# Optimization experiments

Hardware: AMD Instinct MI355X
Metric: run time of the kernel (lower is better)

## Reference

```python
import jax, jax.numpy as jnp
import numpy as np
from jax import lax

B_, DIM, H, W, Dd = 2, 256, 16, 16, 16
DI, N, DTR, K = 256, 8, 16, 4   # d_inner (expand=1), d_state, dt_rank=ceil(256/16), d_conv
OUT_C = 1200
L = H * W * Dd
EPS = 1e-5


def setup_inputs() -> dict:
    key = jax.random.key(0)
    ks = jax.random.split(key, 20)
    g = lambda k, s: jax.random.normal(k, s, jnp.float32) * 0.02
    A_log = jnp.log(jnp.broadcast_to(jnp.arange(1, N + 1, dtype=jnp.float32), (DI, N)))
    dt_bias = jnp.full((DI,), float(np.log(np.expm1(0.01))), jnp.float32)
    return {
        "input0": jax.random.normal(ks[0], (B_, DIM, H, W, Dd), jnp.float32),
        "input1": jax.random.normal(ks[1], (B_, DIM, H, W, Dd), jnp.float32),
        "norm0_w": jnp.ones((DIM,), jnp.float32),
        "norm0_b": jnp.zeros((DIM,), jnp.float32),
        "norm1_w": jnp.ones((DIM,), jnp.float32),
        "norm1_b": jnp.zeros((DIM,), jnp.float32),
        "in_proj_w": g(ks[2], (DI, DIM)),
        "in_projz_w": g(ks[3], (DI, DIM)),
        "conv1d_w": g(ks[4], (DI, 1, K)),
        "conv1d_bias": jnp.zeros((DI,), jnp.float32),
        "conv1db_w": g(ks[5], (DI, 1, K)),
        "conv1db_bias": jnp.zeros((DI,), jnp.float32),
        "xproj_w": g(ks[6], (DTR + 2 * N, DI)),
        "xprojb_w": g(ks[7], (DTR + 2 * N, DI)),
        "dtproj_w": g(ks[8], (DI, DTR)),
        "dtproj_bias": dt_bias,
        "dtprojb_w": g(ks[9], (DI, DTR)),
        "dtprojb_bias": dt_bias,
        "A_log": A_log,
        "Ab_log": A_log,
        "D_p": jnp.ones((DI,), jnp.float32),
        "D_b": jnp.ones((DI,), jnp.float32),
        "rms_w": jnp.ones((DI,), jnp.float32),
        "out_proj_w": g(ks[10], (DIM, DI)),
        "conv3d_w": g(ks[11], (OUT_C, DIM)),
        "conv3d_bias": jnp.zeros((OUT_C,), jnp.float32),
    }


def _layernorm(x, w, b):
    m = x.mean(-1, keepdims=True)
    v = ((x - m) ** 2).mean(-1, keepdims=True)
    return (x - m) * lax.rsqrt(v + EPS) * w + b


def _rmsnorm(x, w):
    return x * lax.rsqrt((x * x).mean(-1, keepdims=True) + EPS) * w


def _ssm_dir(x, z, conv_w, conv_b, xproj_w, dtproj_w, dtproj_bias, A_log, Dp):
    # One direction of the bimamba-v2 selective scan. x, z: (b, L, d_inner)
    xt = x.transpose(0, 2, 1)  # (b, d, L)
    xc = lax.conv_general_dilated(xt, conv_w, (1,), [(K - 1, 0)], feature_group_count=DI)
    x = jax.nn.silu(xc + conv_b[None, :, None]).transpose(0, 2, 1)  # causal dw-conv + silu
    dbl = x @ xproj_w.T                                   # (b, L, dt_rank + 2n)
    dt, Bm, Cm = dbl[..., :DTR], dbl[..., DTR:DTR + N], dbl[..., DTR + N:]
    dt = jax.nn.softplus(dt @ dtproj_w.T + dtproj_bias)    # (b, L, d)
    A = -jnp.exp(A_log)                                    # (d, n)
    dA = jnp.exp(dt[..., None] * A)                        # (b, L, d, n)
    dBu = (dt * x)[..., None] * Bm[:, :, None, :]          # (b, L, d, n)

    def step(h, inp):
        dA_t, dBu_t, C_t = inp
        h = h * dA_t + dBu_t
        return h, jnp.einsum('bdn,bn->bd', h, C_t)

    h0 = jnp.zeros((x.shape[0], DI, N), x.dtype)
    _, ys = lax.scan(step, h0, (dA.transpose(1, 0, 2, 3), dBu.transpose(1, 0, 2, 3), Cm.transpose(1, 0, 2)))
    y = ys.transpose(1, 0, 2) + x * Dp                     # (b, L, d)
    return y * jax.nn.silu(z)                              # gate from the matching branch


def _forward(input0, input1, norm0_w, norm0_b, norm1_w, norm1_b, in_proj_w, in_projz_w,
             conv1d_w, conv1d_bias, conv1db_w, conv1db_bias, xproj_w, xprojb_w,
             dtproj_w, dtproj_bias, dtprojb_w, dtprojb_bias, A_log, Ab_log,
             D_p, D_b, rms_w, out_proj_w, conv3d_w, conv3d_bias):
    b = input0.shape[0]
    skip = input0
    seq0 = input0.transpose(0, 2, 3, 4, 1).reshape(b, L, DIM)  # b (h w d) c
    seq1 = input1.transpose(0, 2, 3, 4, 1).reshape(b, L, DIM)
    seq0 = _layernorm(seq0, norm0_w, norm0_b)
    seq1 = _layernorm(seq1, norm1_w, norm1_b)
    x = seq0 @ in_proj_w.T    # SSM input from input0
    z = seq1 @ in_projz_w.T   # gate from extra_emb (input1)
    y_f = _ssm_dir(x, z, conv1d_w, conv1d_bias, xproj_w, dtproj_w, dtproj_bias, A_log, D_p)
    y_b = _ssm_dir(x[:, ::-1], z[:, ::-1], conv1db_w, conv1db_bias, xprojb_w,
                   dtprojb_w, dtprojb_bias, Ab_log, D_b)[:, ::-1]

    def head(y):
        o = _rmsnorm(y, rms_w) @ out_proj_w.T              # use_norm=True, then out_proj
        o = o.reshape(b, H, W, Dd, DIM).transpose(0, 4, 1, 2, 3) + skip
        return jnp.einsum('bchwd,oc->bohwd', o, conv3d_w) + conv3d_bias[None, :, None, None, None]

    out = head((y_f + y_b) * 0.5)   # if_devide_out=True
    return out, head(y_f), head(y_b)


def reference(input0, input1, norm0_w, norm0_b, norm1_w, norm1_b, in_proj_w, in_projz_w,
              conv1d_w, conv1d_bias, conv1db_w, conv1db_bias, xproj_w, xprojb_w,
              dtproj_w, dtproj_bias, dtprojb_w, dtprojb_bias, A_log, Ab_log,
              D_p, D_b, rms_w, out_proj_w, conv3d_w, conv3d_bias):
    return _forward(input0, input1, norm0_w, norm0_b, norm1_w, norm1_b, in_proj_w, in_projz_w,
                    conv1d_w, conv1d_bias, conv1db_w, conv1db_bias, xproj_w, xprojb_w,
                    dtproj_w, dtproj_bias, dtprojb_w, dtprojb_bias, A_log, Ab_log,
                    D_p, D_b, rms_w, out_proj_w, conv3d_w, conv3d_bias)
```

## Files before the change

### kernel.cpp

```cpp
#include <hip/hip_runtime.h>
#include <cstdint>

#define NTOK 8192

typedef __attribute__((ext_vector_type(4))) float f32x4;
typedef __attribute__((ext_vector_type(8))) short s16x8;
typedef __attribute__((ext_vector_type(4))) short s16x4;

__device__ __forceinline__ short f2bf(float f) {
  union { float f; unsigned u; } x; x.f = f;
  unsigned r = x.u + 0x7FFFu + ((x.u >> 16) & 1u);
  return (short)(r >> 16);
}
__device__ __forceinline__ float bf2f(short s) {
  union { float f; unsigned u; } x;
  x.u = ((unsigned)(unsigned short)s) << 16;
  return x.f;
}
__device__ __forceinline__ void gl_lds16(const void* g, void* l) {
  __builtin_amdgcn_global_load_lds((const unsigned int*)g, (unsigned int*)l, 16, 0, 0);
}

__global__ __launch_bounds__(256) void ln_transpose_kernel(
    const float* __restrict__ in0, const float* __restrict__ in1,
    const float* __restrict__ w0, const float* __restrict__ b0,
    const float* __restrict__ w1, const float* __restrict__ b1,
    const float* __restrict__ wxp, const float* __restrict__ wzp,
    const float* __restrict__ wop, const float* __restrict__ wcp,
    short* __restrict__ Wx, short* __restrict__ Wz,
    short* __restrict__ Wo, short* __restrict__ Wc,
    short* __restrict__ xlnz)
{
  __shared__ float tile[32 * 257];
  __shared__ float mu[32], rs[32];
  const int tid  = threadIdx.x;
  const int pass = blockIdx.x >> 8;
  const int b    = (blockIdx.x >> 7) & 1;
  const int l0   = (blockIdx.x & 127) << 5;

  {
    int base = (int)blockIdx.x << 10;
    #pragma unroll
    for (int i = 0; i < 4; ++i) {
      int idx = base + (i << 8) + tid;
      if (idx < 65536)       Wx[idx] = f2bf(wxp[idx]);
      else if (idx < 131072) Wz[idx - 65536] = f2bf(wzp[idx - 65536]);
      else if (idx < 196608) Wo[idx - 131072] = f2bf(wop[idx - 131072]);
      else {
        int k = idx - 196608;
        Wc[k] = ((k >> 8) < 1200) ? f2bf(wcp[k]) : (short)0;
      }
    }
  }

  const float* in = pass ? in1 : in0;
  #pragma unroll 8
  for (int i = 0; i < 32; ++i) {
    int e = (i << 8) + tid;
    int c = e >> 5, lo = e & 31;
    tile[lo * 257 + c] = in[((size_t)(b * 256 + c) << 12) + l0 + lo];
  }
  __syncthreads();
  if (tid < 64) {
    int r = tid & 31, hh = tid >> 5;
    float s = 0.f, ss = 0.f;
    #pragma unroll 16
    for (int c = hh * 128; c < hh * 128 + 128; ++c) {
      float v = tile[r * 257 + c];
      s += v; ss += v * v;
    }
    s  += __shfl_xor(s, 32, 64);
    ss += __shfl_xor(ss, 32, 64);
    if (hh == 0) {
      float m = s * (1.f / 256.f);
      mu[r] = m;
      rs[r] = rsqrtf(ss * (1.f / 256.f) - m * m + 1e-5f);
    }
  }
  __syncthreads();
  const float* w  = pass ? w1 : w0;
  const float* bb = pass ? b1 : b0;
  float wv = w[tid], bv = bb[tid];
  #pragma unroll 8
  for (int i = 0; i < 32; ++i) {
    float v = tile[i * 257 + tid];
    int row = (pass ? 8192 : 0) + (b << 12) + l0 + i;
    xlnz[(size_t)row * 256 + tid] = f2bf((v - mu[i]) * rs[i] * wv + bv);
  }
}

template <int EPI>
__global__ __launch_bounds__(256) void gemm_fast(
    const short* __restrict__ A, const short* __restrict__ W0,
    const short* __restrict__ W1, float* __restrict__ Cf,
    short* __restrict__ Cb, const float* __restrict__ ADD,
    const float* __restrict__ bias, int Msplit)
{
  __shared__ short As[2][4096];
  __shared__ short Bs[2][4096];
  const int tid  = threadIdx.x;
  const int lane = tid & 63, wave = tid >> 6;
  const int m0 = blockIdx.y << 7;
  const int n0 = blockIdx.x << 7;
  const short* W = (EPI == 0 && m0 >= Msplit) ? W1 : W0;

  const int sr = tid >> 2;
  const int sc = (tid & 3) << 3;
  const int mf = lane & 15, kq = lane >> 4;
  const int wm = (wave & 1) << 6, wn = (wave >> 1) << 6;

  const short* Ar0 = A + (size_t)(m0 + sr) * 256 + sc;
  const short* Ar1 = A + (size_t)(m0 + 64 + sr) * 256 + sc;
  const short* Br0 = W + (size_t)(n0 + sr) * 256 + sc;
  const short* Br1 = W + (size_t)(n0 + 64 + sr) * 256 + sc;
  const int wo = wave << 9;

  f32x4 acc[4][4] = {};

  gl_lds16(Ar0, &As[0][wo]);
  gl_lds16(Ar1, &As[0][wo + 2048]);
  gl_lds16(Br0, &Bs[0][wo]);
  gl_lds16(Br1, &Bs[0][wo + 2048]);
  __syncthreads();

  #pragma unroll
  for (int t = 0; t < 8; ++t) {
    const int cur = t & 1;
    if (t < 7) {
      const int kt = (t + 1) << 5;
      gl_lds16(Ar0 + kt, &As[cur ^ 1][wo]);
      gl_lds16(Ar1 + kt, &As[cur ^ 1][wo + 2048]);
      gl_lds16(Br0 + kt, &Bs[cur ^ 1][wo]);
      gl_lds16(Br1 + kt, &Bs[cur ^ 1][wo + 2048]);
    }
    s16x8 af[4], bfr[4];
    #pragma unroll
    for (int i = 0; i < 4; ++i)
      af[i] = *(const s16x8*)&As[cur][((wm + (i << 4) + mf) << 5) + (kq << 3)];
    #pragma unroll
    for (int j = 0; j < 4; ++j)
      bfr[j] = *(const s16x8*)&Bs[cur][((wn + (j << 4) + mf) << 5) + (kq << 3)];
    #pragma unroll
    for (int i = 0; i < 4; ++i)
      #pragma unroll
      for (int j = 0; j < 4; ++j)
        acc[i][j] = __builtin_amdgcn_mfma_f32_16x16x32_bf16(af[i], bfr[j], acc[i][j], 0, 0, 0);
    __syncthreads();
  }

  if (EPI == 0) {
    #pragma unroll
    for (int i = 0; i < 4; ++i) {
      int gm = m0 + wm + (i << 4) + (kq << 2);
      #pragma unroll
      for (int j = 0; j < 4; ++j) {
        int gn = n0 + wn + (j << 4) + mf;
        #pragma unroll
        for (int r = 0; r < 4; ++r)
          Cf[(size_t)(gm + r) * 256 + gn] = acc[i][j][r];
      }
    }
  } else {
    const int head = m0 >> 13, bb = (m0 >> 12) & 1, lb = m0 & 4095;
    float* obase = Cf + (size_t)head * (2u * 1200u * 4096u) + (size_t)bb * (1200u * 4096u);
    #pragma unroll
    for (int i = 0; i < 4; ++i) {
      int l = lb + wm + (i << 4) + (kq << 2);
      #pragma unroll
      for (int j = 0; j < 4; ++j) {
        int gn = n0 + wn + (j << 4) + mf;
        if (gn < 1200) {
          float bv = bias[gn];
          f32x4 v = acc[i][j];
          v[0] += bv; v[1] += bv; v[2] += bv; v[3] += bv;
          __builtin_nontemporal_store(v, (f32x4*)&obase[(size_t)gn * 4096 + l]);
        }
      }
    }
  }
}

__global__ __launch_bounds__(256) void fused_front(
    const float* __restrict__ x,
    const float* __restrict__ cw0, const float* __restrict__ cb0,
    const float* __restrict__ cw1, const float* __restrict__ cb1,
    const float* __restrict__ xw0, const float* __restrict__ xw1,
    const float* __restrict__ dtw0, const float* __restrict__ dtb0,
    const float* __restrict__ dtw1, const float* __restrict__ dtb1,
    const float* __restrict__ Alog0, const float* __restrict__ Alog1,
    float* __restrict__ xcg, float* __restrict__ dblg,
    float* __restrict__ P, float* __restrict__ Q)
{
  __shared__ float xcs[16 * 256];
  __shared__ short wxs[32 * 264];
  __shared__ float dls[512];
  const int tid = threadIdx.x;
  const int dir = blockIdx.x >> 9;
  const int b   = (blockIdx.x >> 8) & 1;
  const int ch  = blockIdx.x & 255;
  const int t0  = ch << 4;
  const float* cw   = dir ? cw1 : cw0;
  const float* cb   = dir ? cb1 : cb0;
  const float* xw   = dir ? xw1 : xw0;
  const float* dtw  = dir ? dtw1 : dtw0;
  const float* dtb  = dir ? dtb1 : dtb0;
  const float* Alog = dir ? Alog1 : Alog0;
  const size_t dS = (size_t)dir * (NTOK * 256);
  const size_t xb = ((size_t)b) << 12;

  {
    const int d = tid;
    const float w0 = cw[(d << 2)], w1 = cw[(d << 2) + 1],
                w2 = cw[(d << 2) + 2], w3 = cw[(d << 2) + 3];
    const float bias = cb[d];
    float h0 = 0.f, h1 = 0.f, h2 = 0.f;
    #pragma unroll
    for (int i = 0; i < 3; ++i) {
      int ts = t0 - 3 + i; float v = 0.f;
      if (ts >= 0) { int tn = dir ? 4095 - ts : ts; v = x[(xb + tn) * 256 + d]; }
      h0 = h1; h1 = h2; h2 = v;
    }
    #pragma unroll
    for (int s = 0; s < 16; ++s) {
      int ts = t0 + s;
      int tn = dir ? 4095 - ts : ts;
      float xv = x[(xb + tn) * 256 + d];
      float a = bias + w0 * h0 + w1 * h1 + w2 * h2 + w3 * xv;
      h0 = h1; h1 = h2; h2 = xv;
      float v = a / (1.f + __expf(-a));
      xcs[s * 256 + d] = v;
      xcg[dS + (xb + ts) * 256 + d] = v;
    }
  }
  #pragma unroll
  for (int i = 0; i < 32; ++i)
    wxs[i * 264 + tid] = f2bf(xw[(i << 8) + tid]);
  __syncthreads();

  {
    const int j = tid & 31, s0 = tid >> 5;
    float a0 = 0.f, a1 = 0.f;
    const short* wr = &wxs[j * 264];
    const float* xa = &xcs[s0 * 256];
    const float* xbp = &xcs[(s0 + 8) * 256];
    #pragma unroll 4
    for (int rb = 0; rb < 32; ++rb) {
      s16x8 w8 = *(const s16x8*)&wr[rb << 3];
      f32x4 p0 = *(const f32x4*)&xa[rb << 3];
      f32x4 p1 = *(const f32x4*)&xa[(rb << 3) + 4];
      f32x4 q0 = *(const f32x4*)&xbp[rb << 3];
      f32x4 q1 = *(const f32x4*)&xbp[(rb << 3) + 4];
      #pragma unroll
      for (int e = 0; e < 4; ++e) {
        float w = bf2f(w8[e]);
        a0 = fmaf(p0[e], w, a0);
        a1 = fmaf(q0[e], w, a1);
      }
      #pragma unroll
      for (int e = 0; e < 4; ++e) {
        float w = bf2f(w8[4 + e]);
        a0 = fmaf(p1[e], w, a0);
        a1 = fmaf(q1[e], w, a1);
      }
    }
    dls[(s0 << 5) + j] = a0;
    dls[((s0 + 8) << 5) + j] = a1;
    size_t db = (size_t)dir * 262144 + ((xb + t0) << 5);
    dblg[db + tid] = a0;
    dblg[db + 256 + tid] = a1;
  }
  __syncthreads();

  {
    const int d = tid;
    float wrow[16];
    #pragma unroll
    for (int r = 0; r < 16; ++r) wrow[r] = dtw[(d << 4) + r];
    const float bias = dtb[d];
    float Av[8], p[8], q[8];
    #pragma unroll
    for (int n = 0; n < 8; ++n) {
      Av[n] = -expf(Alog[(d << 3) + n]); p[n] = 1.f; q[n] = 0.f;
    }
    for (int s = 0; s < 16; ++s) {
      const float* dlp = &dls[s << 5];
      f32x4 d0 = *(const f32x4*)&dlp[0];
      f32x4 d1 = *(const f32x4*)&dlp[4];
      f32x4 d2 = *(const f32x4*)&dlp[8];
      f32x4 d3 = *(const f32x4*)&dlp[12];
      float a = bias;
      #pragma unroll
      for (int e = 0; e < 4; ++e) a = fmaf(d0[e], wrow[e], a);
      #pragma unroll
      for (int e = 0; e < 4; ++e) a = fmaf(d1[e], wrow[4 + e], a);
      #pragma unroll
      for (int e = 0; e < 4; ++e) a = fmaf(d2[e], wrow[8 + e], a);
      #pragma unroll
      for (int e = 0; e < 4; ++e) a = fmaf(d3[e], wrow[12 + e], a);
      float dtv = (a > 20.f) ? a : log1pf(__expf(a));
      float xv = xcs[s * 256 + d];
      float du = dtv * xv;
      float Bv[8];
      *(f32x4*)&Bv[0] = *(const f32x4*)&dlp[16];
      *(f32x4*)&Bv[4] = *(const f32x4*)&dlp[20];
      #pragma unroll
      for (int n = 0; n < 8; ++n) {
        float dA = __expf(dtv * Av[n]);
        p[n] *= dA;
        q[n] = fmaf(q[n], dA, du * Bv[n]);
      }
    }
    size_t ob = (size_t)dir * 1048576 + ((size_t)((b << 8) + ch) * 8) * 256 + d;
    #pragma unroll
    for (int n = 0; n < 8; ++n) { P[ob + (n << 8)] = p[n]; Q[ob + (n << 8)] = q[n]; }
  }
}

__global__ __launch_bounds__(64) void scan_p2(
    const float* __restrict__ P, const float* __restrict__ Q, float* __restrict__ Hs)
{
  const int d   = ((blockIdx.x & 3) << 6) + threadIdx.x;
  const int bid = blockIdx.x >> 2;
  const int dir = bid >> 4, b = (bid >> 3) & 1, n = bid & 7;
  const size_t dOff = (size_t)dir * 1048576;
  float h = 0.f;
  #pragma unroll 8
  for (int ch = 0; ch < 256; ++ch) {
    size_t i = dOff + ((size_t)((b << 8) + ch) * 8 + n) * 256 + d;
    Hs[i] = h;
    h = fmaf(P[i], h, Q[i]);
  }
}

__global__ __launch_bounds__(256) void scan_p3(
    const float* __restrict__ xcg, const float* __restrict__ dblg,
    const float* __restrict__ dtw0, const float* __restrict__ dtb0,
    const float* __restrict__ dtw1, const float* __restrict__ dtb1,
    const float* __restrict__ Hs, const float* __restrict__ z,
    const float* __restrict__ Alog0, const float* __restrict__ Alog1,
    const float* __restrict__ Dp0, const float* __restrict__ Dp1,
    short* __restrict__ yall)
{
  __shared__ float dl[512];
  const int d = threadIdx.x;
  const int dir = blockIdx.x >> 9;
  const int b   = (blockIdx.x >> 8) & 1;
  const int ch  = blockIdx.x & 255;
  const int t0  = ch << 4;
  const float* dtw  = dir ? dtw1 : dtw0;
  const float* dtb  = dir ? dtb1 : dtb0;
  const float* Alog = dir ? Alog1 : Alog0;
  const float* Dp   = dir ? Dp1 : Dp0;
  const size_t dS = (size_t)dir * (NTOK * 256);
  const size_t xb = ((size_t)b) << 12;
  short* y = yall + (size_t)dir * (NTOK * 256);

  size_t db = (size_t)dir * 262144 + ((xb + t0) << 5);
  dl[d]       = dblg[db + d];
  dl[256 + d] = dblg[db + 256 + d];
  float wrow[16];
  #pragma unroll
  for (int r = 0; r < 16; ++r) wrow[r] = dtw[(d << 4) + r];
  const float bias = dtb[d];
  float Av[8], h[8];
  #pragma unroll
  for (int n = 0; n < 8; ++n) Av[n] = -expf(Alog[(d << 3) + n]);
  size_t hb = (size_t)dir * 1048576 + ((size_t)((b << 8) + ch) * 8) * 256 + d;
  #pragma unroll
  for (int n = 0; n < 8; ++n) h[n] = Hs[hb + (n << 8)];
  const float Dv = Dp[d];
  __syncthreads();
  for (int s = 0; s < 16; ++s) {
    const float* dlp = &dl[s << 5];
    f32x4 d0 = *(const f32x4*)&dlp[0];
    f32x4 d1 = *(const f32x4*)&dlp[4];
    f32x4 d2 = *(const f32x4*)&dlp[8];
    f32x4 d3 = *(const f32x4*)&dlp[12];
    float a = bias;
    #pragma unroll
    for (int e = 0; e < 4; ++e) a = fmaf(d0[e], wrow[e], a);
    #pragma unroll
    for (int e = 0; e < 4; ++e) a = fmaf(d1[e], wrow[4 + e], a);
    #pragma unroll
    for (int e = 0; e < 4; ++e) a = fmaf(d2[e], wrow[8 + e], a);
    #pragma unroll
    for (int e = 0; e < 4; ++e) a = fmaf(d3[e], wrow[12 + e], a);
    float dtv = (a > 20.f) ? a : log1pf(__expf(a));
    int ts = t0 + s;
    float xv = xcg[dS + (xb + ts) * 256 + d];
    float du = dtv * xv;
    float Bv[8], Cv[8];
    *(f32x4*)&Bv[0] = *(const f32x4*)&dlp[16];
    *(f32x4*)&Bv[4] = *(const f32x4*)&dlp[20];
    *(f32x4*)&Cv[0] = *(const f32x4*)&dlp[24];
    *(f32x4*)&Cv[4] = *(const f32x4*)&dlp[28];
    float yv = 0.f;
    #pragma unroll
    for (int n = 0; n < 8; ++n) {
      float dA = __expf(dtv * Av[n]);
      h[n] = fmaf(h[n], dA, du * Bv[n]);
      yv = fmaf(h[n], Cv[n], yv);
    }
    yv = fmaf(xv, Dv, yv);
    int tn = dir ? (4095 - ts) : ts;
    size_t zi = (xb + tn) * 256 + d;
    float zv = z[zi];
    y[zi] = f2bf(yv * zv / (1.f + __expf(-zv)));
  }
}

__global__ __launch_bounds__(256) void gemm_rms_epi1(
    const short* __restrict__ yall, const short* __restrict__ W0,
    const float* __restrict__ rmsw, short* __restrict__ Cb,
    const float* __restrict__ in0)
{
  __shared__ short As[2048];
  __shared__ short Bs[4096];
  __shared__ float scale[64];
  __shared__ float rw[256];
  const int tid  = threadIdx.x;
  const int lane = tid & 63, wave = tid >> 6;
  const int m0 = blockIdx.y << 6;
  const int n0 = blockIdx.x << 7;
  const int mode = m0 >> 13;
  const int tok0 = m0 & 8191;
  const short* yf = yall;
  const short* yb = yall + 2097152;
  const short* ysel = (mode == 1) ? yf : yb;

  rw[tid] = rmsw[tid];

  for (int rr = 0; rr < 16; ++rr) {
    int r = (rr << 2) + wave;
    size_t base = (size_t)(tok0 + r) * 256 + (lane << 2);
    float v0, v1, v2, v3;
    if (mode == 0) {
      s16x4 a = *(const s16x4*)&yf[base];
      s16x4 c = *(const s16x4*)&yb[base];
      v0 = 0.5f * (bf2f(a[0]) + bf2f(c[0]));
      v1 = 0.5f * (bf2f(a[1]) + bf2f(c[1]));
      v2 = 0.5f * (bf2f(a[2]) + bf2f(c[2]));
      v3 = 0.5f * (bf2f(a[3]) + bf2f(c[3]));
    } else {
      s16x4 a = *(const s16x4*)&ysel[base];
      v0 = bf2f(a[0]); v1 = bf2f(a[1]); v2 = bf2f(a[2]); v3 = bf2f(a[3]);
    }
    float ss = v0 * v0 + v1 * v1 + v2 * v2 + v3 * v3;
    #pragma unroll
    for (int o = 32; o > 0; o >>= 1) ss += __shfl_xor(ss, o, 64);
    if (lane == 0) scale[r] = rsqrtf(ss * (1.f / 256.f) + 1e-5f);
  }
  __syncthreads();

  const int sr = tid >> 2;
  const int sc = (tid & 3) << 3;
  const int mf = lane & 15, kq = lane >> 4;
  const int wn = wave << 5;
  const short* Br0 = W0 + (size_t)(n0 + sr) * 256 + sc;
  const short* Br1 = W0 + (size_t)(n0 + 64 + sr) * 256 + sc;
  const int wo = wave << 9;

  const int ar = tid >> 2;
  const int ac = (tid & 3) << 3;
  const size_t abase = (size_t)(tok0 + ar) * 256 + ac;
  const float s_r = scale[ar];

  f32x4 acc[4][2] = {};

  for (int t = 0; t < 8; ++t) {
    const int kt = t << 5;
    {
      s16x8 o0;
      if (mode == 0) {
        s16x8 f0 = *(const s16x8*)&yf[abase + kt];
        s16x8 c0 = *(const s16x8*)&yb[abase + kt];
        #pragma unroll
        for (int e = 0; e < 8; ++e)
          o0[e] = f2bf((0.5f * (bf2f(f0[e]) + bf2f(c0[e])) * s_r) * rw[kt + ac + e]);
      } else {
        s16x8 f0 = *(const s16x8*)&ysel[abase + kt];
        #pragma unroll
        for (int e = 0; e < 8; ++e)
          o0[e] = f2bf((bf2f(f0[e]) * s_r) * rw[kt + ac + e]);
      }
      *(s16x8*)&As[(ar << 5) + ac] = o0;
    }
    gl_lds16(Br0 + kt, &Bs[wo]);
    gl_lds16(Br1 + kt, &Bs[wo + 2048]);
    __syncthreads();
    s16x8 af[4], bfr[2];
    #pragma unroll
    for (int i = 0; i < 4; ++i)
      af[i] = *(const s16x8*)&As[(((i << 4) + mf) << 5) + (kq << 3)];
    #pragma unroll
    for (int j = 0; j < 2; ++j)
      bfr[j] = *(const s16x8*)&Bs[((wn + (j << 4) + mf) << 5) + (kq << 3)];
    #pragma unroll
    for (int i = 0; i < 4; ++i)
      #pragma unroll
      for (int j = 0; j < 2; ++j)
        acc[i][j] = __builtin_amdgcn_mfma_f32_16x16x32_bf16(af[i], bfr[j], acc[i][j], 0, 0, 0);
    __syncthreads();
  }

  #pragma unroll
  for (int i = 0; i < 4; ++i) {
    int gm = m0 + (i << 4) + (kq << 2);
    int tok = gm & 8191;
    int bb2 = tok >> 12, ll = tok & 4095;
    #pragma unroll
    for (int j = 0; j < 2; ++j) {
      int gn = n0 + wn + (j << 4) + mf;
      f32x4 sk = *(const f32x4*)&in0[((((size_t)(bb2 << 8)) + gn) << 12) + ll];
      #pragma unroll
      for (int r = 0; r < 4; ++r) {
        float v = acc[i][j][r] + sk[r];
        Cb[(size_t)(gm + r) * 256 + gn] = f2bf(v);
      }
    }
  }
}

extern "C" void kernel_launch(void* const* d_in, const int* in_sizes, int n_in,
                              void* d_out, int out_size, void* d_ws, size_t ws_size,
                              hipStream_t stream) {
  const float* in0        = (const float*)d_in[0];
  const float* in1        = (const float*)d_in[1];
  const float* n0w        = (const float*)d_in[2];
  const float* n0b        = (const float*)d_in[3];
  const float* n1w        = (const float*)d_in[4];
  const float* n1b        = (const float*)d_in[5];
  const float* in_proj_w  = (const float*)d_in[6];
  const float* in_projz_w = (const float*)d_in[7];
  const float* conv1d_w   = (const float*)d_in[8];
  const float* conv1d_b   = (const float*)d_in[9];
  const float* conv1db_w  = (const float*)d_in[10];
  const float* conv1db_b  = (const float*)d_in[11];
  const float* xproj_w    = (const float*)d_in[12];
  const float* xprojb_w   = (const float*)d_in[13];
  const float* dtproj_w   = (const float*)d_in[14];
  const float* dtproj_b   = (const float*)d_in[15];
  const float* dtprojb_w  = (const float*)d_in[16];
  const float* dtprojb_b  = (const float*)d_in[17];
  const float* A_log      = (const float*)d_in[18];
  const float* Ab_log     = (const float*)d_in[19];
  const float* D_p        = (const float*)d_in[20];
  const float* D_b        = (const float*)d_in[21];
  const float* rms_w      = (const float*)d_in[22];
  const float* out_proj_w = (const float*)d_in[23];
  const float* conv3d_w   = (const float*)d_in[24];
  const float* conv3d_b   = (const float*)d_in[25];
  (void)in_sizes; (void)n_in; (void)out_size; (void)ws_size;

  float* ws = (float*)d_ws;
  size_t o = 0;
  short* xlnz = (short*)(ws + o); o += 2097152;
  float* x    = ws + o;           o += 2097152;
  float* z    = ws + o;           o += 2097152;
  float* xc2  = ws + o;           o += 4194304;
  float* dbl2 = ws + o;           o += 524288;
  float* P    = ws + o;           o += 2097152;
  float* Q    = ws + o;           o += 2097152;
  float* Hs   = ws + o;           o += 2097152;
  short* yall = (short*)(ws + o); o += 2097152;
  short* obuf = (short*)(ws + o); o += 3145728;
  short* Wx   = (short*)(ws + o); o += 32768;
  short* Wz   = (short*)(ws + o); o += 32768;
  short* Wo   = (short*)(ws + o); o += 32768;
  short* Wc   = (short*)(ws + o); o += 163840;
  float* out  = (float*)d_out;

  dim3 blk(256);

  ln_transpose_kernel<<<dim3(512), blk, 0, stream>>>(
      in0, in1, n0w, n0b, n1w, n1b,
      in_proj_w, in_projz_w, out_proj_w, conv3d_w, Wx, Wz, Wo, Wc,
      xlnz);

  gemm_fast<0><<<dim3(2, 128), blk, 0, stream>>>(xlnz, Wx, Wz, x, nullptr, nullptr, nullptr, 8192);

  fused_front<<<dim3(1024), blk, 0, stream>>>(
      x, conv1d_w, conv1d_b, conv1db_w, conv1db_b,
      xproj_w, xprojb_w, dtproj_w, dtproj_b, dtprojb_w, dtprojb_b,
      A_log, Ab_log, xc2, dbl2, P, Q);

  scan_p2<<<dim3(128), dim3(64), 0, stream>>>(P, Q, Hs);

  scan_p3<<<dim3(1024), blk, 0, stream>>>(
      xc2, dbl2, dtproj_w, dtproj_b, dtprojb_w, dtprojb_b,
      Hs, z, A_log, Ab_log, D_p, D_b, yall);

  gemm_rms_epi1<<<dim3(2, 384), blk, 0, stream>>>(yall, Wo, rms_w, obuf, in0);
  gemm_fast<2><<<dim3(10, 192), blk, 0, stream>>>(obuf, Wc, nullptr, out, nullptr, nullptr, conv3d_b, 0);
}
```

Measured before the change: 333.5 us.

## Fuse three RMS-norm heads into one GEMM pass; use smaller M tiles for in_proj

The out_proj GEMM now handles all three heads (averaged, forward, backward) in one block per token tile. It reads yf and yb once, builds three normalized A tiles, and reuses each loaded weight tile across three accumulator sets. Before, three separate row ranges each reloaded y and the weights. The in_proj GEMM is split into a 64-row-tile kernel so the launch has twice as many blocks and fills the CUs better. The cost is higher register and LDS use per block in the fused kernel, which may lower occupancy.

```diff
diff --git a/kernel.cpp b/kernel.cpp
--- a/kernel.cpp
+++ b/kernel.cpp
@@ -89,12 +89,75 @@
   }
 }
 
-template <int EPI>
-__global__ __launch_bounds__(256) void gemm_fast(
+__global__ __launch_bounds__(256) void gemm_in64(
     const short* __restrict__ A, const short* __restrict__ W0,
-    const short* __restrict__ W1, float* __restrict__ Cf,
-    short* __restrict__ Cb, const float* __restrict__ ADD,
-    const float* __restrict__ bias, int Msplit)
+    const short* __restrict__ W1, float* __restrict__ Cf, int Msplit)
+{
+  __shared__ short As[2][2048];
+  __shared__ short Bs[2][4096];
+  const int tid  = threadIdx.x;
+  const int lane = tid & 63, wave = tid >> 6;
+  const int m0 = blockIdx.y << 6;
+  const int n0 = blockIdx.x << 7;
+  const short* W = (m0 >= Msplit) ? W1 : W0;
+
+  const int sr = tid >> 2;
+  const int sc = (tid & 3) << 3;
+  const int mf = lane & 15, kq = lane >> 4;
+  const int wn = wave << 5;
+
+  const short* Ar  = A + (size_t)(m0 + sr) * 256 + sc;
+  const short* Br0 = W + (size_t)(n0 + sr) * 256 + sc;
+  const short* Br1 = W + (size_t)(n0 + 64 + sr) * 256 + sc;
+  const int wo = wave << 9;
+
+  f32x4 acc[4][2] = {};
+
+  gl_lds16(Ar, &As[0][wo]);
+  gl_lds16(Br0, &Bs[0][wo]);
+  gl_lds16(Br1, &Bs[0][wo + 2048]);
+  __syncthreads();
+
+  #pragma unroll
+  for (int t = 0; t < 8; ++t) {
+    const int cur = t & 1;
+    if (t < 7) {
+      const int kt = (t + 1) << 5;
+      gl_lds16(Ar + kt, &As[cur ^ 1][wo]);
+      gl_lds16(Br0 + kt, &Bs[cur ^ 1][wo]);
+      gl_lds16(Br1 + kt, &Bs[cur ^ 1][wo + 2048]);
+    }
+    s16x8 af[4], bfr[2];
+    #pragma unroll
+    for (int i = 0; i < 4; ++i)
+      af[i] = *(const s16x8*)&As[cur][(((i << 4) + mf) << 5) + (kq << 3)];
+    #pragma unroll
+    for (int j = 0; j < 2; ++j)
+      bfr[j] = *(const s16x8*)&Bs[cur][((wn + (j << 4) + mf) << 5) + (kq << 3)];
+    #pragma unroll
+    for (int i = 0; i < 4; ++i)
+      #pragma unroll
+      for (int j = 0; j < 2; ++j)
+        acc[i][j] = __builtin_amdgcn_mfma_f32_16x16x32_bf16(af[i], bfr[j], acc[i][j], 0, 0, 0);
+    __syncthreads();
+  }
+
+  #pragma unroll
+  for (int i = 0; i < 4; ++i) {
+    int gm = m0 + (i << 4) + (kq << 2);
+    #pragma unroll
+    for (int j = 0; j < 2; ++j) {
+      int gn = n0 + wn + (j << 4) + mf;
+      #pragma unroll
+      for (int r = 0; r < 4; ++r)
+        Cf[(size_t)(gm + r) * 256 + gn] = acc[i][j][r];
+    }
+  }
+}
+
+__global__ __launch_bounds__(256) void gemm_conv3d(
+    const short* __restrict__ A, const short* __restrict__ W0,
+    float* __restrict__ Cf, const float* __restrict__ bias)
 {
   __shared__ short As[2][4096];
   __shared__ short Bs[2][4096];
@@ -102,7 +165,6 @@
   const int lane = tid & 63, wave = tid >> 6;
   const int m0 = blockIdx.y << 7;
   const int n0 = blockIdx.x << 7;
-  const short* W = (EPI == 0 && m0 >= Msplit) ? W1 : W0;
 
   const int sr = tid >> 2;
   const int sc = (tid & 3) << 3;
@@ -111,8 +173,8 @@
 
   const short* Ar0 = A + (size_t)(m0 + sr) * 256 + sc;
   const short* Ar1 = A + (size_t)(m0 + 64 + sr) * 256 + sc;
-  const short* Br0 = W + (size_t)(n0 + sr) * 256 + sc;
-  const short* Br1 = W + (size_t)(n0 + 64 + sr) * 256 + sc;
+  const short* Br0 = W0 + (size_t)(n0 + sr) * 256 + sc;
+  const short* Br1 = W0 + (size_t)(n0 + 64 + sr) * 256 + sc;
   const int wo = wave << 9;
 
   f32x4 acc[4][4] = {};
@@ -148,33 +210,19 @@
     __syncthreads();
   }
 
-  if (EPI == 0) {
-    #pragma unroll
-    for (int i = 0; i < 4; ++i) {
-      int gm = m0 + wm + (i << 4) + (kq << 2);
-      #pragma unroll
-      for (int j = 0; j < 4; ++j) {
-        int gn = n0 + wn + (j << 4) + mf;
-        #pragma unroll
-        for (int r = 0; r < 4; ++r)
-          Cf[(size_t)(gm + r) * 256 + gn] = acc[i][j][r];
-      }
-    }
-  } else {
-    const int head = m0 >> 13, bb = (m0 >> 12) & 1, lb = m0 & 4095;
-    float* obase = Cf + (size_t)head * (2u * 1200u * 4096u) + (size_t)bb * (1200u * 4096u);
-    #pragma unroll
-    for (int i = 0; i < 4; ++i) {
-      int l = lb + wm + (i << 4) + (kq << 2);
-      #pragma unroll
-      for (int j = 0; j < 4; ++j) {
-        int gn = n0 + wn + (j << 4) + mf;
-        if (gn < 1200) {
-          float bv = bias[gn];
-          f32x4 v = acc[i][j];
-          v[0] += bv; v[1] += bv; v[2] += bv; v[3] += bv;
-          __builtin_nontemporal_store(v, (f32x4*)&obase[(size_t)gn * 4096 + l]);
-        }
+  const int head = m0 >> 13, bb = (m0 >> 12) & 1, lb = m0 & 4095;
+  float* obase = Cf + (size_t)head * (2u * 1200u * 4096u) + (size_t)bb * (1200u * 4096u);
+  #pragma unroll
+  for (int i = 0; i < 4; ++i) {
+    int l = lb + wm + (i << 4) + (kq << 2);
+    #pragma unroll
+    for (int j = 0; j < 4; ++j) {
+      int gn = n0 + wn + (j << 4) + mf;
+      if (gn < 1200) {
+        float bv = bias[gn];
+        f32x4 v = acc[i][j];
+        v[0] += bv; v[1] += bv; v[2] += bv; v[3] += bv;
+        __builtin_nontemporal_store(v, (f32x4*)&obase[(size_t)gn * 4096 + l]);
       }
     }
   }
@@ -409,46 +457,47 @@
   }
 }
 
-__global__ __launch_bounds__(256) void gemm_rms_epi1(
+__global__ __launch_bounds__(256) void gemm_rms3(
     const short* __restrict__ yall, const short* __restrict__ W0,
     const float* __restrict__ rmsw, short* __restrict__ Cb,
     const float* __restrict__ in0)
 {
-  __shared__ short As[2048];
+  __shared__ short As0[2048], As1[2048], As2[2048];
   __shared__ short Bs[4096];
-  __shared__ float scale[64];
+  __shared__ float sc0[64], sc1[64], sc2[64];
   __shared__ float rw[256];
   const int tid  = threadIdx.x;
   const int lane = tid & 63, wave = tid >> 6;
-  const int m0 = blockIdx.y << 6;
+  const int tok0 = blockIdx.y << 6;
   const int n0 = blockIdx.x << 7;
-  const int mode = m0 >> 13;
-  const int tok0 = m0 & 8191;
   const short* yf = yall;
   const short* yb = yall + 2097152;
-  const short* ysel = (mode == 1) ? yf : yb;
 
   rw[tid] = rmsw[tid];
 
   for (int rr = 0; rr < 16; ++rr) {
     int r = (rr << 2) + wave;
     size_t base = (size_t)(tok0 + r) * 256 + (lane << 2);
-    float v0, v1, v2, v3;
-    if (mode == 0) {
-      s16x4 a = *(const s16x4*)&yf[base];
-      s16x4 c = *(const s16x4*)&yb[base];
-      v0 = 0.5f * (bf2f(a[0]) + bf2f(c[0]));
-      v1 = 0.5f * (bf2f(a[1]) + bf2f(c[1]));
-      v2 = 0.5f * (bf2f(a[2]) + bf2f(c[2]));
-      v3 = 0.5f * (bf2f(a[3]) + bf2f(c[3]));
-    } else {
-      s16x4 a = *(const s16x4*)&ysel[base];
-      v0 = bf2f(a[0]); v1 = bf2f(a[1]); v2 = bf2f(a[2]); v3 = bf2f(a[3]);
-    }
-    float ss = v0 * v0 + v1 * v1 + v2 * v2 + v3 * v3;
-    #pragma unroll
-    for (int o = 32; o > 0; o >>= 1) ss += __shfl_xor(ss, o, 64);
-    if (lane == 0) scale[r] = rsqrtf(ss * (1.f / 256.f) + 1e-5f);
+    s16x4 a = *(const s16x4*)&yf[base];
+    s16x4 c = *(const s16x4*)&yb[base];
+    float f0 = bf2f(a[0]), f1 = bf2f(a[1]), f2 = bf2f(a[2]), f3 = bf2f(a[3]);
+    float g0 = bf2f(c[0]), g1 = bf2f(c[1]), g2 = bf2f(c[2]), g3 = bf2f(c[3]);
+    float h0 = 0.5f * (f0 + g0), h1 = 0.5f * (f1 + g1),
+          h2 = 0.5f * (f2 + g2), h3 = 0.5f * (f3 + g3);
+    float sA = h0 * h0 + h1 * h1 + h2 * h2 + h3 * h3;
+    float sF = f0 * f0 + f1 * f1 + f2 * f2 + f3 * f3;
+    float sB = g0 * g0 + g1 * g1 + g2 * g2 + g3 * g3;
+    #pragma unroll
+    for (int o = 32; o > 0; o >>= 1) {
+      sA += __shfl_xor(sA, o, 64);
+      sF += __shfl_xor(sF, o, 64);
+      sB += __shfl_xor(sB, o, 64);
+    }
+    if (lane == 0) {
+      sc0[r] = rsqrtf(sA * (1.f / 256.f) + 1e-5f);
+      sc1[r] = rsqrtf(sF * (1.f / 256.f) + 1e-5f);
+      sc2[r] = rsqrtf(sB * (1.f / 256.f) + 1e-5f);
+    }
   }
   __syncthreads();
 
@@ -463,50 +512,56 @@
   const int ar = tid >> 2;
   const int ac = (tid & 3) << 3;
   const size_t abase = (size_t)(tok0 + ar) * 256 + ac;
-  const float s_r = scale[ar];
-
-  f32x4 acc[4][2] = {};
+  const float r0 = sc0[ar], r1 = sc1[ar], r2 = sc2[ar];
+
+  f32x4 acc0[4][2] = {}, acc1[4][2] = {}, acc2[4][2] = {};
 
   for (int t = 0; t < 8; ++t) {
     const int kt = t << 5;
     {
-      s16x8 o0;
-      if (mode == 0) {
-        s16x8 f0 = *(const s16x8*)&yf[abase + kt];
-        s16x8 c0 = *(const s16x8*)&yb[abase + kt];
-        #pragma unroll
-        for (int e = 0; e < 8; ++e)
-          o0[e] = f2bf((0.5f * (bf2f(f0[e]) + bf2f(c0[e])) * s_r) * rw[kt + ac + e]);
-      } else {
-        s16x8 f0 = *(const s16x8*)&ysel[abase + kt];
-        #pragma unroll
-        for (int e = 0; e < 8; ++e)
-          o0[e] = f2bf((bf2f(f0[e]) * s_r) * rw[kt + ac + e]);
-      }
-      *(s16x8*)&As[(ar << 5) + ac] = o0;
+      s16x8 f8 = *(const s16x8*)&yf[abase + kt];
+      s16x8 c8 = *(const s16x8*)&yb[abase + kt];
+      s16x8 oA, oF, oB;
+      #pragma unroll
+      for (int e = 0; e < 8; ++e) {
+        float fv = bf2f(f8[e]), cv = bf2f(c8[e]);
+        float w = rw[kt + ac + e];
+        oA[e] = f2bf((0.5f * (fv + cv) * r0) * w);
+        oF[e] = f2bf((fv * r1) * w);
+        oB[e] = f2bf((cv * r2) * w);
+      }
+      *(s16x8*)&As0[(ar << 5) + ac] = oA;
+      *(s16x8*)&As1[(ar << 5) + ac] = oF;
+      *(s16x8*)&As2[(ar << 5) + ac] = oB;
     }
     gl_lds16(Br0 + kt, &Bs[wo]);
     gl_lds16(Br1 + kt, &Bs[wo + 2048]);
     __syncthreads();
-    s16x8 af[4], bfr[2];
-    #pragma unroll
-    for (int i = 0; i < 4; ++i)
-      af[i] = *(const s16x8*)&As[(((i << 4) + mf) << 5) + (kq << 3)];
+    s16x8 a0[4], a1[4], a2[4], bfr[2];
+    #pragma unroll
+    for (int i = 0; i < 4; ++i) {
+      int off = (((i << 4) + mf) << 5) + (kq << 3);
+      a0[i] = *(const s16x8*)&As0[off];
+      a1[i] = *(const s16x8*)&As1[off];
+      a2[i] = *(const s16x8*)&As2[off];
+    }
     #pragma unroll
     for (int j = 0; j < 2; ++j)
       bfr[j] = *(const s16x8*)&Bs[((wn + (j << 4) + mf) << 5) + (kq << 3)];
     #pragma unroll
     for (int i = 0; i < 4; ++i)
       #pragma unroll
-      for (int j = 0; j < 2; ++j)
-        acc[i][j] = __builtin_amdgcn_mfma_f32_16x16x32_bf16(af[i], bfr[j], acc[i][j], 0, 0, 0);
+      for (int j = 0; j < 2; ++j) {
+        acc0[i][j] = __builtin_amdgcn_mfma_f32_16x16x32_bf16(a0[i], bfr[j], acc0[i][j], 0, 0, 0);
+        acc1[i][j] = __builtin_amdgcn_mfma_f32_16x16x32_bf16(a1[i], bfr[j], acc1[i][j], 0, 0, 0);
+        acc2[i][j] = __builtin_amdgcn_mfma_f32_16x16x32_bf16(a2[i], bfr[j], acc2[i][j], 0, 0, 0);
+      }
     __syncthreads();
   }
 
   #pragma unroll
   for (int i = 0; i < 4; ++i) {
-    int gm = m0 + (i << 4) + (kq << 2);
-    int tok = gm & 8191;
+    int tok = tok0 + (i << 4) + (kq << 2);
     int bb2 = tok >> 12, ll = tok & 4095;
     #pragma unroll
     for (int j = 0; j < 2; ++j) {
@@ -514,8 +569,10 @@
       f32x4 sk = *(const f32x4*)&in0[((((size_t)(bb2 << 8)) + gn) << 12) + ll];
       #pragma unroll
       for (int r = 0; r < 4; ++r) {
-        float v = acc[i][j][r] + sk[r];
-        Cb[(size_t)(gm + r) * 256 + gn] = f2bf(v);
+        float s = sk[r];
+        Cb[((size_t)(tok + r)) * 256 + gn]         = f2bf(acc0[i][j][r] + s);
+        Cb[((size_t)(8192 + tok + r)) * 256 + gn]  = f2bf(acc1[i][j][r] + s);
+        Cb[((size_t)(16384 + tok + r)) * 256 + gn] = f2bf(acc2[i][j][r] + s);
       }
     }
   }
@@ -577,7 +634,7 @@
       in_proj_w, in_projz_w, out_proj_w, conv3d_w, Wx, Wz, Wo, Wc,
       xlnz);
 
-  gemm_fast<0><<<dim3(2, 128), blk, 0, stream>>>(xlnz, Wx, Wz, x, nullptr, nullptr, nullptr, 8192);
+  gemm_in64<<<dim3(2, 256), blk, 0, stream>>>(xlnz, Wx, Wz, x, 8192);
 
   fused_front<<<dim3(1024), blk, 0, stream>>>(
       x, conv1d_w, conv1d_b, conv1db_w, conv1db_b,
@@ -590,6 +647,6 @@
       xc2, dbl2, dtproj_w, dtproj_b, dtprojb_w, dtprojb_b,
       Hs, z, A_log, Ab_log, D_p, D_b, yall);
 
-  gemm_rms_epi1<<<dim3(2, 384), blk, 0, stream>>>(yall, Wo, rms_w, obuf, in0);
-  gemm_fast<2><<<dim3(10, 192), blk, 0, stream>>>(obuf, Wc, nullptr, out, nullptr, nullptr, conv3d_b, 0);
-}
+  gemm_rms3<<<dim3(2, 128), blk, 0, stream>>>(yall, Wo, rms_w, obuf, in0);
+  gemm_conv3d<<<dim3(10, 192), blk, 0, stream>>>(obuf, Wc, out, conv3d_b);
+}
```

Result: no change. 335.5 us (+0.6%).
